# Optimization experiments

Measured on AMD Instinct MI355X. Metric: run time of the kernel, lower is better.

The kernel has to match this reference:

```python
import jax, jax.numpy as jnp
import numpy as np

B, T, D, H, O = 128, 1024, 256, 512, 256

def setup_inputs() -> dict:
    key = jax.random.key(0)
    k0, k1, k2, k3 = jax.random.split(key, 4)
    s_i = 1.0 / np.sqrt(D)
    s_h = 1.0 / np.sqrt(H)
    return {
        "X": jax.random.normal(k0, (B, T, D), jnp.float32),
        "Wi": jax.random.normal(k1, (D, 4 * H), jnp.float32) * s_i,  # input kernel (no bias in flax OptimizedLSTMCell input dense)
        "Wh": jax.random.normal(k2, (H, 4 * H), jnp.float32) * s_h,  # recurrent kernel
        "b": jnp.zeros((4 * H,), jnp.float32),                        # recurrent bias
        "Wd": jax.random.normal(k3, (H, O), jnp.float32) * s_h,      # output Dense kernel
        "bd": jnp.zeros((O,), jnp.float32),                           # output Dense bias
    }

def _lstm_last_hidden(X, Wi, Wh, b):
    # Precompute input projections for all timesteps (same linear map, hoisted out of scan)
    x_proj = jnp.einsum('btd,dg->btg', X, Wi)  # [B, T, 4H]
    h_dim = Wh.shape[0]
    c0 = jnp.zeros((X.shape[0], h_dim), X.dtype)
    h0 = c0

    def step(carry, xt):
        c, h = carry
        y = xt + h @ Wh + b  # [B, 4H]
        i, f, g, o = jnp.split(y, 4, axis=-1)  # flax OptimizedLSTMCell gate order: i, f, g, o
        i = jax.nn.sigmoid(i)
        f = jax.nn.sigmoid(f)
        g = jnp.tanh(g)
        o = jax.nn.sigmoid(o)
        c_new = f * c + i * g
        h_new = o * jnp.tanh(c_new)
        return (c_new, h_new), None

    (c_T, h_T), _ = jax.lax.scan(step, (c0, h0), jnp.swapaxes(x_proj, 0, 1))
    return h_T  # [B, H] = last hidden state

def reference(X, Wi, Wh, b, Wd, bd):
    # Original applies Dense to all timesteps then slices [:, -1, :];
    # Dense is pointwise over time, so applying it to the last hidden is identical math.
    h_last = _lstm_last_hidden(X, Wi, Wh, b)
    return h_last @ Wd + bd  # [B, O]
```

## Files before the change

kernel.cpp:

```cpp
#include <hip/hip_runtime.h>
#include <hip/hip_bf16.h>

#define Bb 128
#define Tt 1024
#define Dd 256
#define Hh 512
#define G4 2048
#define Oo 256

#define NBG 8
#define WPB 8
#define NWG_LAUNCH 128
#define BLOCK 512

#define SPIN_CAP (1u << 20)

typedef __attribute__((ext_vector_type(8))) short short8;
typedef __attribute__((ext_vector_type(4))) float f32x4;
typedef unsigned long long u64;

#define TICK_OFF 0
#define CNT_OFF  2048
#define HBUF_OFF 4096
#define WS_ZERO_BYTES (4096 + Bb*Hh*2)

__device__ __forceinline__ short f2bf(float f) {
  __hip_bfloat16 h = __float2bfloat16(f);
  return *reinterpret_cast<short*>(&h);
}
__device__ __forceinline__ float sigm(float x) {
  return __builtin_amdgcn_rcpf(1.f + __expf(-x));
}
__device__ __forceinline__ float tanh_(float x) {
  return fmaf(2.f, __builtin_amdgcn_rcpf(1.f + __expf(-2.f * x)), -1.f);
}

#define MFMA16(A, B, C) __builtin_amdgcn_mfma_f32_16x16x32_bf16((A), (B), (C), 0, 0, 0)

__global__ __launch_bounds__(BLOCK, 2) void lstm_seq(
    const float* __restrict__ X, const float* __restrict__ Wi,
    const float* __restrict__ Wh, const float* __restrict__ bias,
    char* hbuf, int* cnts, int* tickets)
{
  __shared__ char sH[16 * 1024];
  __shared__ char sX[16 * 512];
  __shared__ float sY[8][16][33];
  __shared__ unsigned short hstage[16][72];
  __shared__ int sSlot;

  const int tid  = threadIdx.x;
  const int w    = tid >> 6;
  const int lane = tid & 63;

  int myxcc;
  asm volatile("s_getreg_b32 %0, hwreg(HW_REG_XCC_ID)" : "=s"(myxcc));
  myxcc &= 7;
  if (tid == 0) {
    sSlot = __hip_atomic_fetch_add(&tickets[myxcc * 16], 1,
                                   __ATOMIC_RELAXED, __HIP_MEMORY_SCOPE_AGENT);
  }
  __syncthreads();
  const int gjw = sSlot;
  if (gjw >= WPB) return;
  const int bg = myxcc;
  int* cnt = cnts + bg * 32;

  short8 wf[2][24];
  float bv[2];
#pragma unroll
  for (int nt = 0; nt < 2; ++nt) {
    int c = nt * 16 + (lane & 15);
    int gate = c >> 3, jj0 = c & 7;
    int colg = gate * Hh + gjw * 64 + w * 8 + jj0;
    bv[nt] = bias[colg];
#pragma unroll
    for (int kk = 0; kk < 24; ++kk) {
      short8 f;
#pragma unroll
      for (int i = 0; i < 8; ++i) {
        int k = kk * 32 + (lane >> 4) * 8 + i;
        float v = (k < Hh) ? Wh[(size_t)k * G4 + colg]
                           : Wi[(size_t)(k - Hh) * G4 + colg];
        f[i] = f2bf(v);
      }
      wf[nt][kk] = f;
    }
  }

  const int ejj = lane & 7;
  const int er0 = lane >> 3;
  float cpr[2] = {0.f, 0.f};

  const int arow = lane & 15;
  const int kgrp = lane >> 4;
  const int aswz = (arow & 7) << 4;

  for (int s = 1; s <= Tt; ++s) {
    const char* hread  = hbuf + (size_t)((s - 1) & 1) * (Bb * Hh * 2);
    char*       hwrite = hbuf + (size_t)(s & 1) * (Bb * Hh * 2);

    {
      int row = tid >> 5, seg = tid & 31;
      const float* xp = X + ((size_t)(bg * 16 + row) * Tt + (s - 1)) * Dd + seg * 8;
      f32x4 x0 = *reinterpret_cast<const f32x4*>(xp);
      f32x4 x1 = *reinterpret_cast<const f32x4*>(xp + 4);
      short8 xb;
      xb[0] = f2bf(x0[0]); xb[1] = f2bf(x0[1]); xb[2] = f2bf(x0[2]); xb[3] = f2bf(x0[3]);
      xb[4] = f2bf(x1[0]); xb[5] = f2bf(x1[1]); xb[6] = f2bf(x1[2]); xb[7] = f2bf(x1[3]);
      *reinterpret_cast<short8*>(sX + row * 512 + ((seg * 16) ^ ((row & 7) << 4))) = xb;
    }

    if (s > 1 && tid == 0) {
      const int tgt = WPB * (s - 1);
      unsigned spin = 0;
      while ((int)(__hip_atomic_fetch_add((unsigned*)cnt, 0x10000u,
                                          __ATOMIC_RELAXED,
                                          __HIP_MEMORY_SCOPE_WORKGROUP) & 0xFFFFu) < tgt
             && ++spin < SPIN_CAP) {}
    }
    __syncthreads();

    asm volatile("buffer_inv sc0" ::: "memory");
#pragma unroll
    for (int q = 0; q < 2; ++q) {
      int c = tid + q * 512, row = c >> 6, off = c & 63;
      f32x4 v = *reinterpret_cast<const f32x4*>(
          hread + (size_t)(bg * 16 + row) * 1024 + off * 16);
      *reinterpret_cast<f32x4*>(sH + row * 1024 + ((off * 16) ^ ((row & 7) << 4))) = v;
    }
    __syncthreads();

    f32x4 acc0, acc1;
#pragma unroll
    for (int m = 0; m < 4; ++m) { acc0[m] = bv[0]; acc1[m] = bv[1]; }
#pragma unroll
    for (int kk = 0; kk < 16; ++kk) {
      short8 a = *reinterpret_cast<const short8*>(
          sH + arow * 1024 + ((kk * 64 + kgrp * 16) ^ aswz));
      acc0 = MFMA16(a, wf[0][kk], acc0);
      acc1 = MFMA16(a, wf[1][kk], acc1);
    }
#pragma unroll
    for (int kk = 0; kk < 8; ++kk) {
      short8 a = *reinterpret_cast<const short8*>(
          sX + arow * 512 + ((kk * 64 + kgrp * 16) ^ aswz));
      acc0 = MFMA16(a, wf[0][16 + kk], acc0);
      acc1 = MFMA16(a, wf[1][16 + kk], acc1);
    }

    float* sYw = &sY[w][0][0];
#pragma unroll
    for (int m = 0; m < 4; ++m) {
      int row = kgrp * 4 + m;
      sYw[row * 33 + (lane & 15)]      = acc0[m];
      sYw[row * 33 + 16 + (lane & 15)] = acc1[m];
    }
#pragma unroll
    for (int q = 0; q < 2; ++q) {
      int r = er0 + q * 8;
      float yi = sYw[r * 33 + ejj];
      float yf = sYw[r * 33 + 8 + ejj];
      float yg = sYw[r * 33 + 16 + ejj];
      float yo = sYw[r * 33 + 24 + ejj];
      float ig = sigm(yi), fg = sigm(yf), gg = tanh_(yg), og = sigm(yo);
      float c = fg * cpr[q] + ig * gg;
      cpr[q] = c;
      float hh = og * tanh_(c);
      __hip_bfloat16 hb = __float2bfloat16(hh);
      hstage[r][w * 8 + ejj] = *reinterpret_cast<unsigned short*>(&hb);
    }
    __syncthreads();

    if (tid < 128) {
      int row = tid >> 3, colq = tid & 7;
      f32x4 v = *reinterpret_cast<const f32x4*>(
          reinterpret_cast<const char*>(&hstage[0][0]) + row * 144 + colq * 16);
      *reinterpret_cast<f32x4*>(
          hwrite + ((size_t)(bg * 16 + row) * Hh + gjw * 64 + colq * 8) * 2) = v;
    }
    __syncthreads();

    if (tid == 0) {
      (void)__hip_atomic_fetch_add(cnt, 1, __ATOMIC_RELAXED,
                                   __HIP_MEMORY_SCOPE_WORKGROUP);
    }
  }
}

__global__ void out_dense(const __hip_bfloat16* __restrict__ hT,
                          const float* __restrict__ Wd,
                          const float* __restrict__ bd,
                          float* __restrict__ out)
{
  __shared__ float hrow[Hh];
  int b = blockIdx.x;
  int o = threadIdx.x;
  for (int k = o; k < Hh; k += Oo)
    hrow[k] = __bfloat162float(hT[(size_t)b * Hh + k]);
  __syncthreads();
  float acc = bd[o];
  for (int k = 0; k < Hh; ++k)
    acc = fmaf(hrow[k], Wd[(size_t)k * Oo + o], acc);
  out[(size_t)b * Oo + o] = acc;
}

extern "C" void kernel_launch(void* const* d_in, const int* in_sizes, int n_in,
                              void* d_out, int out_size, void* d_ws, size_t ws_size,
                              hipStream_t stream) {
  (void)in_sizes; (void)n_in; (void)out_size; (void)ws_size;
  const float* X  = (const float*)d_in[0];
  const float* Wi = (const float*)d_in[1];
  const float* Wh = (const float*)d_in[2];
  const float* b  = (const float*)d_in[3];
  const float* Wd = (const float*)d_in[4];
  const float* bd = (const float*)d_in[5];
  float* out = (float*)d_out;

  char* ws = (char*)d_ws;
  int* tickets = (int*)(ws + TICK_OFF);
  int* cnts    = (int*)(ws + CNT_OFF);
  char* hbuf   = ws + HBUF_OFF;

  hipMemsetAsync(d_ws, 0, WS_ZERO_BYTES, stream);
  lstm_seq<<<NWG_LAUNCH, BLOCK, 0, stream>>>(X, Wi, Wh, b, hbuf, cnts, tickets);
  out_dense<<<Bb, Oo, 0, stream>>>((const __hip_bfloat16*)hbuf, Wd, bd, out);
}
```

Measured before the change: 2.753 ms.

## Overlap X-projection MFMAs with h load and do gate math via lane shuffles

Issues the global h loads early and runs the X-part MFMAs before writing h into LDS, so the load latency is hidden behind compute. It replaces the LDS round trip for the gate outputs (sY) and the hstage staging buffer with cross-lane shuffles that put the i/f/g/o values together and pack the bf16 h values. Each wavefront's lane 0 group then writes 16-byte chunks straight to global memory. This removes one __syncthreads and two LDS passes per timestep, in exchange for more complex shuffle logic and more scattered global stores.

```diff
diff --git a/kernel.cpp b/kernel.cpp
--- a/kernel.cpp
+++ b/kernel.cpp
@@ -17,6 +17,7 @@
 
 typedef __attribute__((ext_vector_type(8))) short short8;
 typedef __attribute__((ext_vector_type(4))) float f32x4;
+typedef __attribute__((ext_vector_type(4))) unsigned int u32x4;
 typedef unsigned long long u64;
 
 #define TICK_OFF 0
@@ -44,8 +45,6 @@
 {
   __shared__ char sH[16 * 1024];
   __shared__ char sX[16 * 512];
-  __shared__ float sY[8][16][33];
-  __shared__ unsigned short hstage[16][72];
   __shared__ int sSlot;
 
   const int tid  = threadIdx.x;
@@ -87,13 +86,17 @@
     }
   }
 
-  const int ejj = lane & 7;
-  const int er0 = lane >> 3;
+  const int cjj  = lane & 15;
+  const int kgrp = lane >> 4;
+  const int arow = cjj;
+  const int aswz = (arow & 7) << 4;
+  const int hi8  = (cjj >> 3) & 1;
+  const int jj   = cjj & 7;
+  const int orow = kgrp * 4 + hi8 * 2;
   float cpr[2] = {0.f, 0.f};
 
-  const int arow = lane & 15;
-  const int kgrp = lane >> 4;
-  const int aswz = (arow & 7) << 4;
+  const int hrow0 = tid >> 6,         hoff0 = tid & 63;
+  const int hrow1 = (tid + 512) >> 6, hoff1 = tid & 63;
 
   for (int s = 1; s <= Tt; ++s) {
     const char* hread  = hbuf + (size_t)((s - 1) & 1) * (Bb * Hh * 2);
@@ -121,18 +124,28 @@
     __syncthreads();
 
     asm volatile("buffer_inv sc0" ::: "memory");
-#pragma unroll
-    for (int q = 0; q < 2; ++q) {
-      int c = tid + q * 512, row = c >> 6, off = c & 63;
-      f32x4 v = *reinterpret_cast<const f32x4*>(
-          hread + (size_t)(bg * 16 + row) * 1024 + off * 16);
-      *reinterpret_cast<f32x4*>(sH + row * 1024 + ((off * 16) ^ ((row & 7) << 4))) = v;
-    }
+    f32x4 ht0 = *reinterpret_cast<const f32x4*>(
+        hread + (size_t)(bg * 16 + hrow0) * 1024 + hoff0 * 16);
+    f32x4 ht1 = *reinterpret_cast<const f32x4*>(
+        hread + (size_t)(bg * 16 + hrow1) * 1024 + hoff1 * 16);
+
+    f32x4 acc0, acc1;
+#pragma unroll
+    for (int m = 0; m < 4; ++m) { acc0[m] = bv[0]; acc1[m] = bv[1]; }
+#pragma unroll
+    for (int kk = 0; kk < 8; ++kk) {
+      short8 a = *reinterpret_cast<const short8*>(
+          sX + arow * 512 + ((kk * 64 + kgrp * 16) ^ aswz));
+      acc0 = MFMA16(a, wf[0][16 + kk], acc0);
+      acc1 = MFMA16(a, wf[1][16 + kk], acc1);
+    }
+
+    *reinterpret_cast<f32x4*>(
+        sH + hrow0 * 1024 + ((hoff0 * 16) ^ ((hrow0 & 7) << 4))) = ht0;
+    *reinterpret_cast<f32x4*>(
+        sH + hrow1 * 1024 + ((hoff1 * 16) ^ ((hrow1 & 7) << 4))) = ht1;
     __syncthreads();
 
-    f32x4 acc0, acc1;
-#pragma unroll
-    for (int m = 0; m < 4; ++m) { acc0[m] = bv[0]; acc1[m] = bv[1]; }
 #pragma unroll
     for (int kk = 0; kk < 16; ++kk) {
       short8 a = *reinterpret_cast<const short8*>(
@@ -140,43 +153,56 @@
       acc0 = MFMA16(a, wf[0][kk], acc0);
       acc1 = MFMA16(a, wf[1][kk], acc1);
     }
-#pragma unroll
-    for (int kk = 0; kk < 8; ++kk) {
-      short8 a = *reinterpret_cast<const short8*>(
-          sX + arow * 512 + ((kk * 64 + kgrp * 16) ^ aswz));
-      acc0 = MFMA16(a, wf[0][16 + kk], acc0);
-      acc1 = MFMA16(a, wf[1][16 + kk], acc1);
-    }
-
-    float* sYw = &sY[w][0][0];
+
+    float o0[4], o1[4];
 #pragma unroll
     for (int m = 0; m < 4; ++m) {
-      int row = kgrp * 4 + m;
-      sYw[row * 33 + (lane & 15)]      = acc0[m];
-      sYw[row * 33 + 16 + (lane & 15)] = acc1[m];
-    }
+      o0[m] = __shfl_xor(acc0[m], 8);
+      o1[m] = __shfl_xor(acc1[m], 8);
+    }
+    float hv[2];
 #pragma unroll
     for (int q = 0; q < 2; ++q) {
-      int r = er0 + q * 8;
-      float yi = sYw[r * 33 + ejj];
-      float yf = sYw[r * 33 + 8 + ejj];
-      float yg = sYw[r * 33 + 16 + ejj];
-      float yo = sYw[r * 33 + 24 + ejj];
-      float ig = sigm(yi), fg = sigm(yf), gg = tanh_(yg), og = sigm(yo);
+      int m = hi8 * 2 + q;
+      float iv = hi8 ? o0[m]   : acc0[m];
+      float fv = hi8 ? acc0[m] : o0[m];
+      float gv = hi8 ? o1[m]   : acc1[m];
+      float ov = hi8 ? acc1[m] : o1[m];
+      float ig = sigm(iv), fg = sigm(fv), gg = tanh_(gv), og = sigm(ov);
       float c = fg * cpr[q] + ig * gg;
       cpr[q] = c;
-      float hh = og * tanh_(c);
-      __hip_bfloat16 hb = __float2bfloat16(hh);
-      hstage[r][w * 8 + ejj] = *reinterpret_cast<unsigned short*>(&hb);
-    }
-    __syncthreads();
-
-    if (tid < 128) {
-      int row = tid >> 3, colq = tid & 7;
-      f32x4 v = *reinterpret_cast<const f32x4*>(
-          reinterpret_cast<const char*>(&hstage[0][0]) + row * 144 + colq * 16);
-      *reinterpret_cast<f32x4*>(
-          hwrite + ((size_t)(bg * 16 + row) * Hh + gjw * 64 + colq * 8) * 2) = v;
+      hv[q] = og * tanh_(c);
+    }
+
+    {
+      __hip_bfloat16 hb0 = __float2bfloat16(hv[0]);
+      __hip_bfloat16 hb1 = __float2bfloat16(hv[1]);
+      unsigned p0 = (unsigned)*reinterpret_cast<unsigned short*>(&hb0);
+      unsigned p1 = (unsigned)*reinterpret_cast<unsigned short*>(&hb1);
+      unsigned q0 = __shfl_xor(p0, 1), q1 = __shfl_xor(p1, 1);
+      unsigned lo, hi;
+      lo = (jj & 1) ? q0 : p0; hi = (jj & 1) ? p0 : q0;
+      p0 = (lo & 0xFFFFu) | (hi << 16);
+      lo = (jj & 1) ? q1 : p1; hi = (jj & 1) ? p1 : q1;
+      p1 = (lo & 0xFFFFu) | (hi << 16);
+      unsigned r0 = __shfl_xor(p0, 2), r1 = __shfl_xor(p1, 2);
+      unsigned a0 = (jj & 2) ? r0 : p0, a1 = (jj & 2) ? p0 : r0;
+      unsigned b0 = (jj & 2) ? r1 : p1, b1 = (jj & 2) ? p1 : r1;
+      unsigned s0 = __shfl_xor(a0, 4), s1 = __shfl_xor(a1, 4);
+      unsigned t0 = __shfl_xor(b0, 4), t1 = __shfl_xor(b1, 4);
+      u32x4 v0, v1;
+      if ((jj & 4) == 0) {
+        v0[0] = a0; v0[1] = a1; v0[2] = s0; v0[3] = s1;
+        v1[0] = b0; v1[1] = b1; v1[2] = t0; v1[3] = t1;
+      } else {
+        v0[0] = s0; v0[1] = s1; v0[2] = a0; v0[3] = a1;
+        v1[0] = t0; v1[1] = t1; v1[2] = b0; v1[3] = b1;
+      }
+      if (jj == 0) {
+        char* hw = hwrite + ((size_t)(bg * 16 + orow) * Hh + gjw * 64 + w * 8) * 2;
+        *reinterpret_cast<u32x4*>(hw) = v0;
+        *reinterpret_cast<u32x4*>(hw + Hh * 2) = v1;
+      }
     }
     __syncthreads();
 
```

Measured after the change: 3.608 ms. +31.0%, slower.

## Split recurrence across 16 workgroups per batch group with shuffle-based gate exchange

Applied to the files above, without the earlier changes.

Doubles the number of workgroups cooperating on each batch group from 8 to 16, so each wave computes 4 hidden units (one 16-column MFMA tile) instead of 8, halving the per-step MFMA chain and the register-resident weight slice. The gate values for a hidden unit are gathered with cross-lane shuffles instead of going through an LDS transpose buffer, which removes one shared-memory round trip. In exchange, twice as many workgroups must arrive at the per-step global counter barrier, only a quarter of the lanes do the gate math, and the 256 workgroups must all be co-resident for the spin barrier to make progress.

```diff
diff --git a/kernel.cpp b/kernel.cpp
--- a/kernel.cpp
+++ b/kernel.cpp
@@ -9,8 +9,8 @@
 #define Oo 256
 
 #define NBG 8
-#define WPB 8
-#define NWG_LAUNCH 128
+#define WPB 16
+#define NWG_LAUNCH 256
 #define BLOCK 512
 
 #define SPIN_CAP (1u << 20)
@@ -44,8 +44,7 @@
 {
   __shared__ char sH[16 * 1024];
   __shared__ char sX[16 * 512];
-  __shared__ float sY[8][16][33];
-  __shared__ unsigned short hstage[16][72];
+  __shared__ unsigned short hstage[16][40];
   __shared__ int sSlot;
 
   const int tid  = threadIdx.x;
@@ -65,35 +64,30 @@
   const int bg = myxcc;
   int* cnt = cnts + bg * 32;
 
-  short8 wf[2][24];
-  float bv[2];
-#pragma unroll
-  for (int nt = 0; nt < 2; ++nt) {
-    int c = nt * 16 + (lane & 15);
-    int gate = c >> 3, jj0 = c & 7;
-    int colg = gate * Hh + gjw * 64 + w * 8 + jj0;
-    bv[nt] = bias[colg];
-#pragma unroll
-    for (int kk = 0; kk < 24; ++kk) {
-      short8 f;
-#pragma unroll
-      for (int i = 0; i < 8; ++i) {
-        int k = kk * 32 + (lane >> 4) * 8 + i;
-        float v = (k < Hh) ? Wh[(size_t)k * G4 + colg]
-                           : Wi[(size_t)(k - Hh) * G4 + colg];
-        f[i] = f2bf(v);
-      }
-      wf[nt][kk] = f;
-    }
+  const int cjj  = lane & 15;
+  const int kgrp = lane >> 4;
+  const int gate = cjj >> 2;
+  const int c4   = cjj & 3;
+  const int colg = gate * Hh + gjw * 32 + w * 4 + c4;
+
+  short8 wf[24];
+#pragma unroll
+  for (int kk = 0; kk < 24; ++kk) {
+    short8 f;
+#pragma unroll
+    for (int i = 0; i < 8; ++i) {
+      int k = kk * 32 + kgrp * 8 + i;
+      float v = (k < Hh) ? Wh[(size_t)k * G4 + colg]
+                         : Wi[(size_t)(k - Hh) * G4 + colg];
+      f[i] = f2bf(v);
+    }
+    wf[kk] = f;
   }
-
-  const int ejj = lane & 7;
-  const int er0 = lane >> 3;
-  float cpr[2] = {0.f, 0.f};
-
-  const int arow = lane & 15;
-  const int kgrp = lane >> 4;
+  const float bvv = bias[colg];
+
+  const int arow = cjj;
   const int aswz = (arow & 7) << 4;
+  float cpr[4] = {0.f, 0.f, 0.f, 0.f};
 
   for (int s = 1; s <= Tt; ++s) {
     const char* hread  = hbuf + (size_t)((s - 1) & 1) * (Bb * Hh * 2);
@@ -130,53 +124,48 @@
     }
     __syncthreads();
 
-    f32x4 acc0, acc1;
-#pragma unroll
-    for (int m = 0; m < 4; ++m) { acc0[m] = bv[0]; acc1[m] = bv[1]; }
+    f32x4 acc;
+#pragma unroll
+    for (int m = 0; m < 4; ++m) acc[m] = bvv;
 #pragma unroll
     for (int kk = 0; kk < 16; ++kk) {
       short8 a = *reinterpret_cast<const short8*>(
           sH + arow * 1024 + ((kk * 64 + kgrp * 16) ^ aswz));
-      acc0 = MFMA16(a, wf[0][kk], acc0);
-      acc1 = MFMA16(a, wf[1][kk], acc1);
+      acc = MFMA16(a, wf[kk], acc);
     }
 #pragma unroll
     for (int kk = 0; kk < 8; ++kk) {
       short8 a = *reinterpret_cast<const short8*>(
           sX + arow * 512 + ((kk * 64 + kgrp * 16) ^ aswz));
-      acc0 = MFMA16(a, wf[0][16 + kk], acc0);
-      acc1 = MFMA16(a, wf[1][16 + kk], acc1);
-    }
-
-    float* sYw = &sY[w][0][0];
+      acc = MFMA16(a, wf[16 + kk], acc);
+    }
+
+    float r1[4], r2[4], r3[4];
 #pragma unroll
     for (int m = 0; m < 4; ++m) {
-      int row = kgrp * 4 + m;
-      sYw[row * 33 + (lane & 15)]      = acc0[m];
-      sYw[row * 33 + 16 + (lane & 15)] = acc1[m];
-    }
-#pragma unroll
-    for (int q = 0; q < 2; ++q) {
-      int r = er0 + q * 8;
-      float yi = sYw[r * 33 + ejj];
-      float yf = sYw[r * 33 + 8 + ejj];
-      float yg = sYw[r * 33 + 16 + ejj];
-      float yo = sYw[r * 33 + 24 + ejj];
-      float ig = sigm(yi), fg = sigm(yf), gg = tanh_(yg), og = sigm(yo);
-      float c = fg * cpr[q] + ig * gg;
-      cpr[q] = c;
-      float hh = og * tanh_(c);
-      __hip_bfloat16 hb = __float2bfloat16(hh);
-      hstage[r][w * 8 + ejj] = *reinterpret_cast<unsigned short*>(&hb);
-    }
-    __syncthreads();
-
-    if (tid < 128) {
-      int row = tid >> 3, colq = tid & 7;
-      f32x4 v = *reinterpret_cast<const f32x4*>(
-          reinterpret_cast<const char*>(&hstage[0][0]) + row * 144 + colq * 16);
+      r1[m] = __shfl_xor(acc[m], 4);
+      r2[m] = __shfl_xor(acc[m], 8);
+      r3[m] = __shfl_xor(r1[m], 8);
+    }
+    if (cjj < 4) {
+#pragma unroll
+      for (int m = 0; m < 4; ++m) {
+        float ig = sigm(acc[m]), fg = sigm(r1[m]);
+        float gg = tanh_(r2[m]), og = sigm(r3[m]);
+        float c = fg * cpr[m] + ig * gg;
+        cpr[m] = c;
+        float hh = og * tanh_(c);
+        __hip_bfloat16 hb = __float2bfloat16(hh);
+        hstage[kgrp * 4 + m][w * 4 + c4] = *reinterpret_cast<unsigned short*>(&hb);
+      }
+    }
+    __syncthreads();
+
+    if (tid < 64) {
+      int row = tid >> 2, chunk = tid & 3;
+      f32x4 v = *reinterpret_cast<const f32x4*>(&hstage[row][chunk * 8]);
       *reinterpret_cast<f32x4*>(
-          hwrite + ((size_t)(bg * 16 + row) * Hh + gjw * 64 + colq * 8) * 2) = v;
+          hwrite + ((size_t)(bg * 16 + row) * Hh + gjw * 32 + chunk * 8) * 2) = v;
     }
     __syncthreads();
 
```

Result: faster. 2.685 ms (-2.5%).
